# Kernel tuning notes

Measured on AMD Instinct MI355X. Metric: run time of the kernel, lower is better.

## Reference

```python
import jax, jax.numpy as jnp
import numpy as np

N_LEVELS = 4
F_DIM = 2
B = 1_000_000
SIZES = [12 * ((2 ** (l - 1)) ** 2 + 2) for l in range(1, N_LEVELS + 1)]  # [36, 72, 216, 792]
MAX_SIZE = max(SIZES)  # 792
NPIX = [12 * (2 ** i) ** 2 for i in range(N_LEVELS)]  # [12, 48, 192, 768]


def setup_inputs() -> dict:
    key = jax.random.key(0)
    ks = jax.random.split(key, 6)
    # learned table, init uniform(-1e-4, 1e-4) as in the torch module
    params = jax.random.uniform(ks[0], (N_LEVELS, MAX_SIZE, F_DIM),
                                minval=-1e-4, maxval=1e-4, dtype=jnp.float32)
    # per-level HEALPix pixel indices, each in [0, npix_level)
    pixel_index = jnp.stack([
        jax.random.randint(jax.random.fold_in(ks[1], i), (B,), 0, NPIX[i], dtype=jnp.int32)
        for i in range(N_LEVELS)])
    neigh = jnp.stack([
        jax.random.randint(jax.random.fold_in(ks[2], i), (8, B), 0, NPIX[i], dtype=jnp.int32)
        for i in range(N_LEVELS)])
    drop = jax.random.uniform(ks[3], (N_LEVELS, 8, B)) < 0.05
    neigh_index = jnp.where(drop, jnp.int32(-1), neigh)
    # latlon in radians: theta in [0, pi], phi in [0, 2*pi)
    u_p = jax.random.uniform(ks[4], (N_LEVELS, B, 2))
    pixel_latlon = jnp.stack([u_p[..., 0] * jnp.pi, u_p[..., 1] * (2 * jnp.pi)], axis=-1).astype(jnp.float32)
    u_n = jax.random.uniform(ks[5], (N_LEVELS, 8 * B, 2))
    neigh_latlon = jnp.stack([u_n[..., 0] * jnp.pi, u_n[..., 1] * (2 * jnp.pi)], axis=-1).astype(jnp.float32)
    return {"params": params, "pixel_latlon": pixel_latlon, "neigh_latlon": neigh_latlon,
            "pixel_index": pixel_index, "neigh_index": neigh_index}


def reference(params, pixel_latlon, neigh_latlon, pixel_index, neigh_index):
    L, _, F = params.shape  # [L, max_size, F]
    Bp = pixel_index.shape[1]
    # index_preprocessing: -1 -> max(index)+1, build keep-mask
    nflat = neigh_index.reshape(L, -1)  # [L, 8B]
    miss = nflat == -1
    nflat = jnp.where(miss, nflat.max() + 1, nflat)
    nmask = (~miss).astype(params.dtype)  # [L, 8B]
    pidx = jnp.where(pixel_index == -1, pixel_index.max() + 1, pixel_index)  # [L, B]
    # gathers from the parameter table
    neigh_reps = jnp.take_along_axis(params, nflat[..., None], axis=1)   # [L, 8B, F]
    my_reps = jnp.take_along_axis(params, pidx[..., None], axis=1)       # [L, B, F]
    # inverse-distance weights (equirectangular "great circle" per source)
    my_ll = jnp.broadcast_to(pixel_latlon[:, None], (L, 8, Bp, 2)).reshape(L, 8 * Bp, 2)
    d = jnp.sqrt((neigh_latlon[..., 1] - my_ll[..., 1]) ** 2 +
                 (neigh_latlon[..., 0] - my_ll[..., 0]) ** 2)  # [L, 8B]
    d = jnp.where(jnp.isinf(d), d.min(), d)
    w = 1.0 / d
    # weight, mask, sum over 8 neighbors, add residual
    out = (neigh_reps * w[..., None]).reshape(L, 8, Bp, F) * nmask.reshape(L, 8, Bp)[..., None]
    out = out.sum(axis=1) + my_reps  # [L, B, F]
    # faithful to torch: reshape(4, -1).t().reshape(-1, L*F)
    out = out.reshape(4, -1).T.reshape(-1, L * F)
    return out.astype(jnp.float32)
```

## Files before the change

kernel.cpp:

```cpp
#include <hip/hip_runtime.h>


#define NLEV 4
#define MAXSZ 792
#define TABSZ (NLEV * MAXSZ * 2)
#define PPB 64

__global__ __launch_bounds__(256, 6) void heal_encoding_kernel(
    const float* __restrict__ params,
    const float* __restrict__ pixel_latlon,
    const float* __restrict__ neigh_latlon,
    const int*   __restrict__ pixel_index,
    const int*   __restrict__ neigh_index,
    float* __restrict__ out,
    int B, int ntiles)
{
    __shared__ float stab[TABSZ];

    const int tid = threadIdx.x;
    const int bl  = tid >> 2;
    const int l   = tid & 3;

    {
        const float4* p4  = (const float4*)params;
        float4*       st4 = (float4*)stab;
        for (int i = tid; i < TABSZ / 4; i += 256)
            st4[i] = p4[i];
    }
    __syncthreads();

    const float2* sp2  = (const float2*)stab;
    const float2* pll2 = (const float2*)pixel_latlon;
    const float2* nll2 = (const float2*)neigh_latlon;
    const int lb = l * MAXSZ;
    const int pb = l * B;
    const int nb = l * 8 * B;

    for (int t = blockIdx.x; t < ntiles; t += gridDim.x) {
        const int b_raw = t * PPB + bl;
        const int b = min(b_raw, B - 1);

        const int    pi  = pixel_index[pb + b];
        const float2 pll = pll2[pb + b];
        int    ni[8];
        float2 nl[8];
        #pragma unroll
        for (int j = 0; j < 8; ++j) {
            ni[j] = neigh_index[nb + j * B + b];
            nl[j] = nll2[nb + j * B + b];
        }

        float a0 = 0.0f, a1 = 0.0f;
        #pragma unroll
        for (int j = 0; j < 8; ++j) {
            float dth = nl[j].x - pll.x;
            float dph = nl[j].y - pll.y;
            float d   = sqrtf(dth * dth + dph * dph);
            float w   = (ni[j] >= 0) ? (1.0f / d) : 0.0f;
            float2 r  = sp2[lb + (ni[j] >= 0 ? ni[j] : 0)];
            a0 += w * r.x;
            a1 += w * r.y;
        }
        float2 m = sp2[lb + (pi < 0 ? 768 : pi)];
        a0 += m.x;
        a1 += m.y;

        const bool odd = (l & 1);
        float x = __shfl_xor(odd ? a0 : a1, 1);
        float2 st = odd ? make_float2(x, a1)
                        : make_float2(a0, x);
        const int col = odd ? (l + 3) : l;
        if (b_raw < B)
            *(float2*)(out + (size_t)b_raw * 8 + col) = st;
    }
}

extern "C" void kernel_launch(void* const* d_in, const int* in_sizes, int n_in,
                              void* d_out, int out_size, void* d_ws, size_t ws_size,
                              hipStream_t stream) {
    const float* params       = (const float*)d_in[0];
    const float* pixel_latlon = (const float*)d_in[1];
    const float* neigh_latlon = (const float*)d_in[2];
    const int*   pixel_index  = (const int*)d_in[3];
    const int*   neigh_index  = (const int*)d_in[4];
    float* out = (float*)d_out;

    int B = in_sizes[3] / NLEV;
    int ntiles = (B + PPB - 1) / PPB;
    int blocks = 1536;
    if (blocks > ntiles) blocks = ntiles;
    heal_encoding_kernel<<<blocks, 256, 0, stream>>>(
        params, pixel_latlon, neigh_latlon, pixel_index, neigh_index, out, B, ntiles);
}
```

Baseline: 470.6 us.

## Double-buffer global loads across grid-stride iterations in software pipeline

The grid-stride loop becomes a software pipeline with two register buffers, so the next tile's index and lat/lon loads are issued before the current tile is computed. This is meant to hide global-memory latency behind the compute and LDS gathers. It roughly doubles live registers, so the launch bound drops from 6 to 4 waves per SIMD and the grid shrinks from 1536 to 1024 blocks, giving up occupancy-based latency hiding. The prefetch at the tail issues redundant loads of the clamped last tile.

```diff
diff --git a/kernel.cpp b/kernel.cpp
--- a/kernel.cpp
+++ b/kernel.cpp
@@ -6,7 +6,45 @@
 #define TABSZ (NLEV * MAXSZ * 2)
 #define PPB 64
 
-__global__ __launch_bounds__(256, 6) void heal_encoding_kernel(
+#define ISSUE_LOADS(pi_, pll_, ni_, nl_, tt)                  \
+    {                                                         \
+        const int b_ = min((tt) * PPB + bl, B - 1);           \
+        pi_  = pixel_index[pb + b_];                          \
+        pll_ = pll2[pb + b_];                                 \
+        _Pragma("unroll")                                     \
+        for (int j = 0; j < 8; ++j) {                         \
+            ni_[j] = neigh_index[nb + j * B + b_];            \
+            nl_[j] = nll2[nb + j * B + b_];                   \
+        }                                                     \
+    }
+
+#define COMPUTE_STORE(pi_, pll_, ni_, nl_, tt)                \
+    {                                                         \
+        float a0 = 0.0f, a1 = 0.0f;                           \
+        _Pragma("unroll")                                     \
+        for (int j = 0; j < 8; ++j) {                         \
+            float dth = nl_[j].x - pll_.x;                    \
+            float dph = nl_[j].y - pll_.y;                    \
+            float d   = sqrtf(dth * dth + dph * dph);         \
+            float w   = (ni_[j] >= 0) ? (1.0f / d) : 0.0f;    \
+            float2 r  = sp2[lb + (ni_[j] >= 0 ? ni_[j] : 0)]; \
+            a0 += w * r.x;                                    \
+            a1 += w * r.y;                                    \
+        }                                                     \
+        float2 m = sp2[lb + (pi_ < 0 ? 768 : pi_)];           \
+        a0 += m.x;                                            \
+        a1 += m.y;                                            \
+        const bool odd = (l & 1);                             \
+        float x = __shfl_xor(odd ? a0 : a1, 1);               \
+        float2 st = odd ? make_float2(x, a1)                  \
+                        : make_float2(a0, x);                 \
+        const int col = odd ? (l + 3) : l;                    \
+        const int bo = (tt) * PPB + bl;                       \
+        if (bo < B)                                           \
+            *(float2*)(out + (size_t)bo * 8 + col) = st;      \
+    }
+
+__global__ __launch_bounds__(256, 4) void heal_encoding_kernel(
     const float* __restrict__ params,
     const float* __restrict__ pixel_latlon,
     const float* __restrict__ neigh_latlon,
@@ -36,42 +74,27 @@
     const int pb = l * B;
     const int nb = l * 8 * B;
 
-    for (int t = blockIdx.x; t < ntiles; t += gridDim.x) {
-        const int b_raw = t * PPB + bl;
-        const int b = min(b_raw, B - 1);
+    const int g    = gridDim.x;
+    const int tmax = ntiles - 1;
+    const int iters = (ntiles - blockIdx.x + g - 1) / g;
 
-        const int    pi  = pixel_index[pb + b];
-        const float2 pll = pll2[pb + b];
-        int    ni[8];
-        float2 nl[8];
-        #pragma unroll
-        for (int j = 0; j < 8; ++j) {
-            ni[j] = neigh_index[nb + j * B + b];
-            nl[j] = nll2[nb + j * B + b];
-        }
+    int piA; float2 pllA; int niA[8]; float2 nlA[8];
+    int piB; float2 pllB; int niB[8]; float2 nlB[8];
 
-        float a0 = 0.0f, a1 = 0.0f;
-        #pragma unroll
-        for (int j = 0; j < 8; ++j) {
-            float dth = nl[j].x - pll.x;
-            float dph = nl[j].y - pll.y;
-            float d   = sqrtf(dth * dth + dph * dph);
-            float w   = (ni[j] >= 0) ? (1.0f / d) : 0.0f;
-            float2 r  = sp2[lb + (ni[j] >= 0 ? ni[j] : 0)];
-            a0 += w * r.x;
-            a1 += w * r.y;
-        }
-        float2 m = sp2[lb + (pi < 0 ? 768 : pi)];
-        a0 += m.x;
-        a1 += m.y;
+    int t = blockIdx.x;
+    ISSUE_LOADS(piA, pllA, niA, nlA, t);
 
-        const bool odd = (l & 1);
-        float x = __shfl_xor(odd ? a0 : a1, 1);
-        float2 st = odd ? make_float2(x, a1)
-                        : make_float2(a0, x);
-        const int col = odd ? (l + 3) : l;
-        if (b_raw < B)
-            *(float2*)(out + (size_t)b_raw * 8 + col) = st;
+    for (int i = 0; i < iters; i += 2) {
+        const int t1 = min(t + g, tmax);
+        ISSUE_LOADS(piB, pllB, niB, nlB, t1);
+        COMPUTE_STORE(piA, pllA, niA, nlA, t);
+
+        const int t2 = min(t1 + g, tmax);
+        ISSUE_LOADS(piA, pllA, niA, nlA, t2);
+        if (i + 1 < iters)
+            COMPUTE_STORE(piB, pllB, niB, nlB, t + g);
+
+        t += 2 * g;
     }
 }
 
@@ -87,7 +110,7 @@
 
     int B = in_sizes[3] / NLEV;
     int ntiles = (B + PPB - 1) / PPB;
-    int blocks = 1536;
+    int blocks = 1024;
     if (blocks > ntiles) blocks = ntiles;
     heal_encoding_kernel<<<blocks, 256, 0, stream>>>(
         params, pixel_latlon, neigh_latlon, pixel_index, neigh_index, out, B, ntiles);
```

Measured after the change: 470.7 us. About the same (+0.0%).
